# Performance work log

Hardware: AMD Instinct MI355X
Metric: run time of the kernel (lower is better)

The kernel has to match this reference:

```python
import jax, jax.numpy as jnp
import numpy as np

N_ATOM = 30000
N_PAIR = 1_000_000
N_TRI = 4_000_000
N_SF = 16
RC = 6.0

LAMBD = jnp.array([-1.0, 1.0] * 8, dtype=jnp.float32)
ZETA = jnp.array([1.0, 1.0, 2.0, 2.0, 4.0, 4.0, 8.0, 8.0] * 2, dtype=jnp.float32)
ETA = jnp.array([0.01, 0.014, 0.02, 0.028, 0.04, 0.056, 0.08, 0.11,
                 0.16, 0.22, 0.32, 0.45, 0.63, 0.72, 0.9, 1.0], dtype=jnp.float32)


def cutoff_f1(r):
    # PiNN 'f1' cutoff: 0.5*(cos(pi*r/rc)+1)
    return 0.5 * (jnp.cos(jnp.float32(np.pi) * r / RC) + 1.0)


def gaussian_basis(r, fc):
    # GaussianBasis with center=0, gamma=eta: fc * exp(-eta * r^2), shape [n, n_sf]
    return fc[:, None] * jnp.exp(-ETA[None, :] * (r[:, None] ** 2))


def setup_inputs() -> dict:
    key = jax.random.key(0)
    k1, k2, k3, k4, k5 = jax.random.split(key, 5)
    ind_2 = jax.random.randint(k1, (N_PAIR, 2), 0, N_ATOM, dtype=jnp.int32)
    ind_3 = jax.random.randint(k2, (N_TRI, 2), 0, N_PAIR, dtype=jnp.int32)
    dist = jax.random.uniform(k3, (N_PAIR,), jnp.float32, 0.5, RC)
    dirs = jax.random.normal(k4, (N_PAIR, 3), jnp.float32)
    dirs = dirs / jnp.linalg.norm(dirs, axis=1, keepdims=True)
    diff = dirs * dist[:, None]  # bond vectors consistent with dist
    elems = jax.random.randint(k5, (N_ATOM,), 0, 4, dtype=jnp.int32)
    fc = cutoff_f1(dist)
    return {"ind_2": ind_2, "ind_3": ind_3, "dist": dist, "diff": diff,
            "elems": elems, "fc": fc}


def reference(ind_2, ind_3, dist, diff, elems, fc):
    # i=j=k='ALL': species filter is identity; a_rind = arange(n_atom)
    ind_ij = ind_3[:, 0]
    ind_ik = ind_3[:, 1]
    i_rind = ind_2[ind_ij, 0]  # central atom index per triplet

    diff_ij = diff[ind_ij]  # [T,3]
    diff_ik = diff[ind_ik]
    diff_jk = diff_ik - diff_ij
    dist_jk = jnp.linalg.norm(diff_jk, axis=1)
    mask = dist_jk < RC  # TF filters triplets; we mask (jit-friendly)

    fc_jk = cutoff_f1(dist_jk)
    dist_ij = dist[ind_ij]
    dist_ik = dist[ind_ik]
    fc_ij = fc[ind_ij]
    fc_ik = fc[ind_ik]

    cos_ijk = jnp.einsum('id,id->i', diff_ij, diff_ik) / dist_ij / dist_ik
    base = jnp.maximum(1.0 + LAMBD[None, :] * cos_ijk[:, None], 0.0)
    sf = (2.0 ** (1.0 - ZETA[None, :]) * base ** ZETA[None, :]
          * gaussian_basis(dist_ij, fc_ij)
          * gaussian_basis(dist_ik, fc_ik)
          * gaussian_basis(dist_jk, fc_jk))
    sf = jnp.where(mask[:, None], sf, 0.0)

    # scatter_nd add into per-atom fingerprints
    fp = jnp.zeros((N_ATOM, N_SF), dtype=sf.dtype).at[i_rind].add(sf)

    # jacobian indices: central-atom rel index per participating pair
    vals = jnp.where(mask, i_rind, -1)
    seg = jnp.concatenate([ind_ij, ind_ik])
    pair_i = jax.ops.segment_max(jnp.concatenate([vals, vals]), seg,
                                 num_segments=N_PAIR)
    pair_i = jnp.maximum(pair_i, -1)  # empty segments -> -1 sentinel
    jacob_ind = jnp.stack([jnp.arange(N_PAIR, dtype=jnp.int32), pair_i], axis=1)
    return fp, jacob_ind
```

## Files before the change

kernel.cpp:

```cpp
#include <hip/hip_runtime.h>

#define N_ATOM 30000
#define N_PAIR 1000000
#define N_TRI  4000000
#define N_SF   16
#define FP_ELEMS (N_ATOM * N_SF)

#define ASH  5
#define APB  32
#define NCB  938
#define NSUB 8
#define NSEG (NCB * NSUB)
#define OVF_CNT_IDX NSEG
#define OVF_CAP 131072
#define TILE 4096
#define PER_TH 16
#define NTILES ((N_TRI + TILE - 1) / TILE)
#define WCAP 1280
#define MERGE 4
#define NRB (NCB * 2)

#define OFF_CCNT   0ULL
#define OFF_PCNT   32768ULL
#define OFF_PPLACE 98304ULL
#define OFF_PBASE  163840ULL
#define OFF_AMAP   196608ULL
#define OFF_FLAGB  4196608ULL
#define OFF_OVF    4327680ULL
#define OFF_PACKS  5376256ULL
#define OFF_CB     21376256ULL
#define ZERO_INTS  41984
#define FLAGB_INTS 32768

__device__ __constant__ float c_eta[16] = {
    0.01f, 0.014f, 0.02f, 0.028f, 0.04f, 0.056f, 0.08f, 0.11f,
    0.16f, 0.22f, 0.32f, 0.45f, 0.63f, 0.72f, 0.9f, 1.0f};

__device__ __forceinline__ bool tri_math(
    float4 A, float4 B, float A8[8], float& R2)
{
    float ax = A.x, ay = A.y, az = A.z;
    float bx = B.x, by = B.y, bz = B.z;
    float d2ij = fmaf(ax, ax, fmaf(ay, ay, az * az));
    float d2ik = fmaf(bx, bx, fmaf(by, by, bz * bz));
    float jx = bx - ax, jy = by - ay, jz = bz - az;
    float d2jk = fmaf(jx, jx, fmaf(jy, jy, jz * jz));
    if (!(d2jk < 36.0f)) return false;
    float dij = sqrtf(d2ij);
    float dik = sqrtf(d2ik);
    float djk = sqrtf(d2jk);
    const float PI_OVER_RC = 0.5235987755982988f;
    float fcij = 0.5f * (__cosf(PI_OVER_RC * dij) + 1.0f);
    float fcik = 0.5f * (__cosf(PI_OVER_RC * dik) + 1.0f);
    float fcjk = 0.5f * (__cosf(PI_OVER_RC * djk) + 1.0f);
    float dot = fmaf(ax, bx, fmaf(ay, by, az * bz));
    float cosv = dot / (dij * dik);
    R2 = d2ij + d2ik + d2jk;
    float FCt = fcij * fcik * fcjk;
    float bm = fmaxf(1.0f - cosv, 0.0f);
    float bp = fmaxf(1.0f + cosv, 0.0f);
    float bm2 = bm * bm, bp2 = bp * bp;
    float bm4 = bm2 * bm2, bp4 = bp2 * bp2;
    float bm8 = bm4 * bm4, bp8 = bp4 * bp4;
    A8[0] = FCt * bm;               A8[1] = FCt * bp;
    A8[2] = 0.5f * FCt * bm2;       A8[3] = 0.5f * FCt * bp2;
    A8[4] = 0.125f * FCt * bm4;     A8[5] = 0.125f * FCt * bp4;
    A8[6] = 0.0078125f * FCt * bm8; A8[7] = 0.0078125f * FCt * bp8;
    return true;
}


__global__ __launch_bounds__(256) void zero_meta(
    int* __restrict__ m, unsigned int* __restrict__ fb)
{
    int i = blockIdx.x * blockDim.x + threadIdx.x;
    if (i < ZERO_INTS) m[i] = 0;
    if (i < FLAGB_INTS) fb[i] = 0u;
}

__global__ __launch_bounds__(256) void pair_hist(
    const int2* __restrict__ ind2, int* __restrict__ pcnt)
{
    __shared__ int h[NCB];
    for (int i = threadIdx.x; i < NCB; i += 256) h[i] = 0;
    __syncthreads();
    int stride = gridDim.x * 256;
    for (int p = blockIdx.x * 256 + threadIdx.x; p < N_PAIR; p += stride)
        atomicAdd(&h[ind2[p].x >> ASH], 1);
    __syncthreads();
    for (int i = threadIdx.x; i < NCB; i += 256) {
        int v = h[i];
        if (v) atomicAdd(&pcnt[i * 16], v);
    }
}

__global__ __launch_bounds__(1024) void scan_bases(
    const int* __restrict__ pcnt, int* __restrict__ pbase)
{
    __shared__ int s[1024];
    int t = threadIdx.x;
    int v0 = (t < NCB) ? pcnt[t * 16] : 0;
    s[t] = v0;
    __syncthreads();
    for (int off = 1; off < 1024; off <<= 1) {
        int v = 0;
        if (t >= off) v = s[t - off];
        __syncthreads();
        s[t] += v;
        __syncthreads();
    }
    if (t < NCB) pbase[t] = s[t] - v0;
    if (t == 0) pbase[NCB] = N_PAIR;
}

__global__ __launch_bounds__(256) void pair_place(
    const int2* __restrict__ ind2, const float* __restrict__ diff,
    const int* __restrict__ pbase, int* __restrict__ pplace,
    unsigned int* __restrict__ amap, float4* __restrict__ packs,
    float* __restrict__ out)
{
    int p = blockIdx.x * blockDim.x + threadIdx.x;
    if (p < FP_ELEMS) out[p] = 0.0f;
    if (p >= N_PAIR) return;
    int a = ind2[p].x;
    int c = a >> ASH;
    int l = atomicAdd(&pplace[c * 16], 1);
    int q = pbase[c] + l;
    amap[p] = ((unsigned)c << 22) | ((unsigned)(a & (APB - 1)) << 17) | (unsigned)l;
    float4 r;
    r.x = diff[3 * p + 0];
    r.y = diff[3 * p + 1];
    r.z = diff[3 * p + 2];
    r.w = __int_as_float(-1);
    packs[q] = r;
}

__global__ __launch_bounds__(256) void bin3(
    const int2* __restrict__ ind3, const unsigned int* __restrict__ amap,
    const int* __restrict__ pbase,
    int* __restrict__ ccnt, int2* __restrict__ cbucket,
    int2* __restrict__ ovf, int cap)
{
    __shared__ int lcnt[NCB];
    __shared__ int lbase[NCB];
    const int thr = threadIdx.x;
    const int sub = blockIdx.x & (NSUB - 1);
    const long long t0 = (long long)blockIdx.x * TILE;

    for (int i = thr; i < NCB; i += 256) lcnt[i] = 0;
    __syncthreads();

    unsigned int mij_r[PER_TH];
    int qik_r[PER_TH];
    int slot_r[PER_TH];
#pragma unroll
    for (int j = 0; j < PER_TH; ++j) {
        long long t = t0 + j * 256 + thr;
        unsigned int mij = 0; int qik = 0, s = -1;
        if (t < N_TRI) {
            int2 pr = ind3[t];
            mij = amap[pr.x];
            unsigned int mik = amap[pr.y];
            qik = pbase[mik >> 22] + (int)(mik & 0x1FFFF);
            s = atomicAdd(&lcnt[mij >> 22], 1);
        }
        mij_r[j] = mij; qik_r[j] = qik; slot_r[j] = s;
    }
    __syncthreads();
    for (int c = thr; c < NCB; c += 256) {
        int n = lcnt[c];
        lbase[c] = n ? atomicAdd(&ccnt[c * NSUB + sub], n) : 0;
    }
    __syncthreads();
#pragma unroll
    for (int j = 0; j < PER_TH; ++j) {
        long long t = t0 + j * 256 + thr;
        if (t >= N_TRI) continue;
        unsigned int mij = mij_r[j];
        int c = mij >> 22;
        int slot = lbase[c] + slot_r[j];
        if (slot < cap) {
            int2 e;
            e.x = (int)(mij & 0x3FFFFF);
            e.y = qik_r[j];
            cbucket[(size_t)(c * NSUB + sub) * cap + slot] = e;
        } else {
            int o = atomicAdd(&ccnt[OVF_CNT_IDX], 1);
            if (o < OVF_CAP) { int2 e; e.x = (int)mij; e.y = qik_r[j]; ovf[o] = e; }
        }
    }
}

__global__ __launch_bounds__(256) void reduce4(
    const int* __restrict__ ccnt, const int2* __restrict__ cbucket, int cap,
    float4* __restrict__ packs, const int* __restrict__ pbase,
    unsigned int* __restrict__ flagbits, float* __restrict__ out)
{
    __shared__ float4 win[WCAP];
    __shared__ float lacc[APB * 17];
    __shared__ unsigned int lflag[WCAP / 32];
    const int blk = blockIdx.x;
    const int b = blk >> 1;
    const int half = blk & 1;
    const int thr = threadIdx.x;
    const int base = pbase[b];
    const int wlen = min(pbase[b + 1] - base, WCAP);

    for (int i = thr; i < APB * 17; i += 256) lacc[i] = 0.0f;
    if (thr < WCAP / 32) lflag[thr] = 0u;
    for (int i = thr; i < wlen; i += 256) win[i] = packs[base + i];

    const int seg0 = b * NSUB + half * MERGE;
    int n0 = min(ccnt[seg0 + 0], cap);
    int n1 = min(ccnt[seg0 + 1], cap);
    int n2 = min(ccnt[seg0 + 2], cap);
    int n3 = min(ccnt[seg0 + 3], cap);
    int c1 = n0, c2 = n0 + n1, c3 = n0 + n1 + n2;
    int m = c3 + n3;
    const int2* segp0 = cbucket + (size_t)seg0 * cap;
    int* pw = (int*)packs;
    __syncthreads();

#define FETCH_E(jj, dst) { \
        int s2_ = (jj >= c1) + (jj >= c2) + (jj >= c3); \
        int o_ = jj - (s2_ == 0 ? 0 : (s2_ == 1 ? c1 : (s2_ == 2 ? c2 : c3))); \
        dst = segp0[(size_t)s2_ * cap + o_]; }

    int j = thr;
    int2 e = make_int2(0, 0);
    float4 B = make_float4(0.f, 0.f, 0.f, 0.f);
    if (j < m) { FETCH_E(j, e); B = packs[e.y]; }
    while (j < m) {
        int jn = j + 256;
        int2 en = make_int2(0, 0);
        float4 Bn = B;
        if (jn < m) { FETCH_E(jn, en); Bn = packs[en.y]; }
        int lidx = e.x & 0x1FFFF;
        int a5 = (e.x >> 17) & (APB - 1);
        float4 A = (lidx < WCAP) ? win[lidx] : packs[base + lidx];
        float A8[8], R2;
        if (tri_math(A, B, A8, R2)) {
            if (lidx < WCAP) {
                atomicOr(&lflag[lidx >> 5], 1u << (lidx & 31));
            } else {
                int g = base + lidx;
                atomicOr(&flagbits[g >> 5], 1u << (g & 31));
            }
            atomicMax(&pw[4 * e.y + 3], (b << ASH) + a5);
#pragma unroll
            for (int s = 0; s < 16; ++s)
                atomicAdd(&lacc[a5 * 17 + s], A8[s & 7] * __expf(-c_eta[s] * R2));
        }
        j = jn; e = en; B = Bn;
    }
#undef FETCH_E
    __syncthreads();

    {
        int sh = base & 31;
        int w0 = base >> 5;
        int nw = (wlen + 31) >> 5;
        for (int i = thr; i < nw; i += 256) {
            unsigned int w = lflag[i];
            if (!w) continue;
            atomicOr(&flagbits[w0 + i], w << sh);
            if (sh) {
                unsigned int hi = w >> (32 - sh);
                if (hi) atomicOr(&flagbits[w0 + i + 1], hi);
            }
        }
    }
    for (int t = thr; t < APB * N_SF; t += 256) {
        int atom = (b << ASH) + (t >> 4);
        float v = lacc[(t >> 4) * 17 + (t & 15)];
        if (atom < N_ATOM && v != 0.0f)
            unsafeAtomicAdd(out + (size_t)atom * N_SF + (t & 15), v);
    }
}

__global__ __launch_bounds__(256) void ovf3(
    const int* __restrict__ ccnt, const int2* __restrict__ ovf,
    float4* __restrict__ packs, const int* __restrict__ pbase,
    unsigned int* __restrict__ flagbits, float* __restrict__ out)
{
    int i = blockIdx.x * blockDim.x + threadIdx.x;
    int n = ccnt[OVF_CNT_IDX];
    if (n > OVF_CAP) n = OVF_CAP;
    if (i >= n) return;
    int2 e = ovf[i];
    unsigned int mij = (unsigned int)e.x;
    int qik = e.y;
    int c = mij >> 22;
    int a5 = (mij >> 17) & (APB - 1);
    int lidx = mij & 0x1FFFF;
    int qij = pbase[c] + lidx;
    float4 A = packs[qij];
    float4 B = packs[qik];
    float A8[8], R2;
    if (!tri_math(A, B, A8, R2)) return;
    int atom = (c << ASH) + a5;
    int* pw = (int*)packs;
    atomicOr(&flagbits[qij >> 5], 1u << (qij & 31));
    atomicMax(&pw[4 * qik + 3], atom);
    float* basep = out + (size_t)atom * N_SF;
#pragma unroll
    for (int s = 0; s < 16; ++s)
        unsafeAtomicAdd(basep + s, A8[s & 7] * __expf(-c_eta[s] * R2));
}

__global__ __launch_bounds__(256) void fin3(
    const unsigned int* __restrict__ amap, const int* __restrict__ pbase,
    const float4* __restrict__ packs, const unsigned int* __restrict__ flagbits,
    float* __restrict__ out)
{
    int p = blockIdx.x * blockDim.x + threadIdx.x;
    if (p >= N_PAIR) return;
    unsigned int mm = amap[p];
    int c = mm >> 22;
    int lidx = (int)(mm & 0x1FFFF);
    int a5 = (mm >> 17) & (APB - 1);
    int q = pbase[c] + lidx;
    int w = ((const int*)packs)[4 * q + 3];
    unsigned int fb = flagbits[q >> 5];
    int a = (c << ASH) + a5;
    int v = ((fb >> (q & 31)) & 1u) ? max(w, a) : w;
    float* jf = out + FP_ELEMS;
    jf[2 * p + 0] = (float)p;
    jf[2 * p + 1] = (float)v;
}


__global__ __launch_bounds__(256) void init_legacy(float* __restrict__ out) {
    int i = blockIdx.x * blockDim.x + threadIdx.x;
    if (i < FP_ELEMS) out[i] = 0.0f;
    if (i < N_PAIR) ((int*)out + FP_ELEMS)[2 * i + 1] = -1;
}

__global__ __launch_bounds__(256) void tri_legacy(
    const int* __restrict__ ind2, const int2* __restrict__ ind3,
    const float* __restrict__ dist, const float* __restrict__ diff,
    const float* __restrict__ fc, float* __restrict__ out) {
    int t = blockIdx.x * blockDim.x + threadIdx.x;
    if (t >= N_TRI) return;
    int2 pr = ind3[t];
    int ij = pr.x, ik = pr.y;
    float4 A, B;
    A.x = diff[3 * ij + 0]; A.y = diff[3 * ij + 1]; A.z = diff[3 * ij + 2]; A.w = 0.f;
    B.x = diff[3 * ik + 0]; B.y = diff[3 * ik + 1]; B.z = diff[3 * ik + 2]; B.w = 0.f;
    float A8[8], R2;
    if (!tri_math(A, B, A8, R2)) return;
    int atom = ind2[2 * ij];
    int* jac = (int*)out + FP_ELEMS;
    atomicMax(&jac[2 * ij + 1], atom);
    atomicMax(&jac[2 * ik + 1], atom);
    float* base = out + (size_t)atom * N_SF;
#pragma unroll
    for (int s = 0; s < 16; ++s)
        unsafeAtomicAdd(base + s, A8[s & 7] * __expf(-c_eta[s] * R2));
}

__global__ __launch_bounds__(256) void fin_legacy(float* __restrict__ out) {
    int p = blockIdx.x * blockDim.x + threadIdx.x;
    if (p >= N_PAIR) return;
    int* jac = (int*)out + FP_ELEMS;
    int v = jac[2 * p + 1];
    float* jf = (float*)jac;
    jf[2 * p + 0] = (float)p;
    jf[2 * p + 1] = (float)v;
}


extern "C" void kernel_launch(void* const* d_in, const int* in_sizes, int n_in,
                              void* d_out, int out_size, void* d_ws, size_t ws_size,
                              hipStream_t stream) {
    const int2*  ind2 = (const int2*)d_in[0];
    const int2*  ind3 = (const int2*)d_in[1];
    const float* dist = (const float*)d_in[2];
    const float* diff = (const float*)d_in[3];
    const float* fc   = (const float*)d_in[5];
    float* out = (float*)d_out;

    const size_t seg_stride = (size_t)NSEG * sizeof(int2);
    const size_t need_min = OFF_CB + seg_stride * 608;

    if (ws_size >= need_min) {
        char* ws = (char*)d_ws;
        int* ccnt            = (int*)(ws + OFF_CCNT);
        int* pcnt            = (int*)(ws + OFF_PCNT);
        int* pplace          = (int*)(ws + OFF_PPLACE);
        int* pbase           = (int*)(ws + OFF_PBASE);
        unsigned int* amap   = (unsigned int*)(ws + OFF_AMAP);
        unsigned int* flagb  = (unsigned int*)(ws + OFF_FLAGB);
        int2* ovf            = (int2*)(ws + OFF_OVF);
        float4* packs        = (float4*)(ws + OFF_PACKS);
        int2* cbucket        = (int2*)(ws + OFF_CB);
        int cap = (int)((ws_size - OFF_CB) / seg_stride);
        if (cap > 1024) cap = 1024;

        int pb = (N_PAIR + 255) / 256;
        zero_meta<<<(ZERO_INTS + 255) / 256, 256, 0, stream>>>((int*)ws, flagb);
        pair_hist<<<240, 256, 0, stream>>>(ind2, pcnt);
        scan_bases<<<1, 1024, 0, stream>>>(pcnt, pbase);
        pair_place<<<pb, 256, 0, stream>>>(ind2, diff, pbase, pplace, amap, packs, out);
        bin3<<<NTILES, 256, 0, stream>>>(ind3, amap, pbase, ccnt, cbucket, ovf, cap);
        reduce4<<<NRB, 256, 0, stream>>>(ccnt, cbucket, cap, packs, pbase, flagb, out);
        ovf3<<<OVF_CAP / 256, 256, 0, stream>>>(ccnt, ovf, packs, pbase, flagb, out);
        fin3<<<pb, 256, 0, stream>>>(amap, pbase, packs, flagb, out);
    } else {
        init_legacy<<<(N_PAIR + 255) / 256, 256, 0, stream>>>(out);
        tri_legacy<<<(N_TRI + 255) / 256, 256, 0, stream>>>((const int*)d_in[0], ind3, dist, diff, fc, out);
        fin_legacy<<<(N_PAIR + 255) / 256, 256, 0, stream>>>(out);
    }
    (void)dist; (void)fc; (void)in_sizes; (void)n_in; (void)out_size;
}
```

Baseline: 552.1 us.

## Split reduce blocks four ways per atom bucket and drop shared pair window

The reduction kernel now launches four blocks per atom bucket, each merging two sub-segments instead of two blocks merging four. The per-block shared-memory copy of the pair-pack window is removed, and A operands are read directly from global memory. The loop is restructured to issue two independent triplets per thread per iteration instead of a software-pipelined prefetch. This cuts LDS use and the window-load prologue and raises block count and occupancy, at the cost of more global A reads and more atomic flushes of lacc into the output.

```diff
diff --git a/kernel.cpp b/kernel.cpp
--- a/kernel.cpp
+++ b/kernel.cpp
@@ -16,9 +16,9 @@
 #define TILE 4096
 #define PER_TH 16
 #define NTILES ((N_TRI + TILE - 1) / TILE)
-#define WCAP 1280
-#define MERGE 4
-#define NRB (NCB * 2)
+#define MERGE 2
+#define NRB (NCB * 4)
+#define LFB 2048
 
 #define OFF_CCNT   0ULL
 #define OFF_PCNT   32768ULL
@@ -196,70 +196,68 @@
     float4* __restrict__ packs, const int* __restrict__ pbase,
     unsigned int* __restrict__ flagbits, float* __restrict__ out)
 {
-    __shared__ float4 win[WCAP];
     __shared__ float lacc[APB * 17];
-    __shared__ unsigned int lflag[WCAP / 32];
+    __shared__ unsigned int lflag[LFB / 32];
     const int blk = blockIdx.x;
-    const int b = blk >> 1;
-    const int half = blk & 1;
+    const int b = blk >> 2;
+    const int quad = blk & 3;
     const int thr = threadIdx.x;
     const int base = pbase[b];
-    const int wlen = min(pbase[b + 1] - base, WCAP);
+    const int wlen = pbase[b + 1] - base;
 
     for (int i = thr; i < APB * 17; i += 256) lacc[i] = 0.0f;
-    if (thr < WCAP / 32) lflag[thr] = 0u;
-    for (int i = thr; i < wlen; i += 256) win[i] = packs[base + i];
-
-    const int seg0 = b * NSUB + half * MERGE;
-    int n0 = min(ccnt[seg0 + 0], cap);
-    int n1 = min(ccnt[seg0 + 1], cap);
-    int n2 = min(ccnt[seg0 + 2], cap);
-    int n3 = min(ccnt[seg0 + 3], cap);
-    int c1 = n0, c2 = n0 + n1, c3 = n0 + n1 + n2;
-    int m = c3 + n3;
+    if (thr < LFB / 32) lflag[thr] = 0u;
+
+    const int seg0 = b * NSUB + quad * MERGE;
+    const int n0 = min(ccnt[seg0 + 0], cap);
+    const int n1 = min(ccnt[seg0 + 1], cap);
+    const int m = n0 + n1;
     const int2* segp0 = cbucket + (size_t)seg0 * cap;
     int* pw = (int*)packs;
     __syncthreads();
 
-#define FETCH_E(jj, dst) { \
-        int s2_ = (jj >= c1) + (jj >= c2) + (jj >= c3); \
-        int o_ = jj - (s2_ == 0 ? 0 : (s2_ == 1 ? c1 : (s2_ == 2 ? c2 : c3))); \
-        dst = segp0[(size_t)s2_ * cap + o_]; }
-
-    int j = thr;
-    int2 e = make_int2(0, 0);
-    float4 B = make_float4(0.f, 0.f, 0.f, 0.f);
-    if (j < m) { FETCH_E(j, e); B = packs[e.y]; }
-    while (j < m) {
-        int jn = j + 256;
-        int2 en = make_int2(0, 0);
-        float4 Bn = B;
-        if (jn < m) { FETCH_E(jn, en); Bn = packs[en.y]; }
-        int lidx = e.x & 0x1FFFF;
-        int a5 = (e.x >> 17) & (APB - 1);
-        float4 A = (lidx < WCAP) ? win[lidx] : packs[base + lidx];
-        float A8[8], R2;
-        if (tri_math(A, B, A8, R2)) {
-            if (lidx < WCAP) {
-                atomicOr(&lflag[lidx >> 5], 1u << (lidx & 31));
-            } else {
-                int g = base + lidx;
-                atomicOr(&flagbits[g >> 5], 1u << (g & 31));
-            }
-            atomicMax(&pw[4 * e.y + 3], (b << ASH) + a5);
+    for (int j0 = 0; j0 < m; j0 += 512) {
+        int i1 = j0 + thr;
+        int i2 = i1 + 256;
+        bool v1 = i1 < m, v2 = i2 < m;
+        int jc1 = v1 ? i1 : m - 1;
+        int jc2 = v2 ? i2 : m - 1;
+        int s1 = jc1 >= n0, s2 = jc2 >= n0;
+        int2 e1 = segp0[(size_t)s1 * cap + (jc1 - (s1 ? n0 : 0))];
+        int2 e2 = segp0[(size_t)s2 * cap + (jc2 - (s2 ? n0 : 0))];
+        int l1 = e1.x & 0x1FFFF;
+        int l2 = e2.x & 0x1FFFF;
+        float4 B1 = packs[e1.y];
+        float4 B2 = packs[e2.y];
+        float4 A1 = packs[base + l1];
+        float4 A2 = packs[base + l2];
+
+        float A8[8], R2v;
+        if (v1 && tri_math(A1, B1, A8, R2v)) {
+            int a5 = (e1.x >> 17) & (APB - 1);
+            if (l1 < LFB) atomicOr(&lflag[l1 >> 5], 1u << (l1 & 31));
+            else { int g = base + l1; atomicOr(&flagbits[g >> 5], 1u << (g & 31)); }
+            atomicMax(&pw[4 * e1.y + 3], (b << ASH) + a5);
 #pragma unroll
             for (int s = 0; s < 16; ++s)
-                atomicAdd(&lacc[a5 * 17 + s], A8[s & 7] * __expf(-c_eta[s] * R2));
+                atomicAdd(&lacc[a5 * 17 + s], A8[s & 7] * __expf(-c_eta[s] * R2v));
         }
-        j = jn; e = en; B = Bn;
-    }
-#undef FETCH_E
+        if (v2 && tri_math(A2, B2, A8, R2v)) {
+            int a5 = (e2.x >> 17) & (APB - 1);
+            if (l2 < LFB) atomicOr(&lflag[l2 >> 5], 1u << (l2 & 31));
+            else { int g = base + l2; atomicOr(&flagbits[g >> 5], 1u << (g & 31)); }
+            atomicMax(&pw[4 * e2.y + 3], (b << ASH) + a5);
+#pragma unroll
+            for (int s = 0; s < 16; ++s)
+                atomicAdd(&lacc[a5 * 17 + s], A8[s & 7] * __expf(-c_eta[s] * R2v));
+        }
+    }
     __syncthreads();
 
     {
         int sh = base & 31;
         int w0 = base >> 5;
-        int nw = (wlen + 31) >> 5;
+        int nw = (min(wlen, LFB) + 31) >> 5;
         for (int i = thr; i < nw; i += 256) {
             unsigned int w = lflag[i];
             if (!w) continue;
```

Measured after the change: 526.6 us. -4.6%, faster.
